# Optimization experiments

Hardware: AMD Instinct MI355X
Metric: run time of the kernel (lower is better)

## Reference

```python
import jax, jax.numpy as jnp
import numpy as np

TEXT = 226          # text_seq_length
D = 1024            # model / inner dim
HEADS = 16
HD = D // HEADS     # 64
F = 13              # latent frames
FH, FW = 8, 12      # feature h/w = H/8/2, W/8/2
ST = F * FH * FW    # 1248 spatial tokens
S = TEXT + ST       # 1474 full sequence
NEG = -1e9


def sdpa(q, k, v, bias=None):
    # q:[b,h,Q,d] k,v:[b,h,K,d]; math path of F.scaled_dot_product_attention
    scale = 1.0 / jnp.sqrt(jnp.asarray(q.shape[-1], q.dtype))
    s = jnp.einsum('bhqd,bhkd->bhqk', q, k) * scale
    if bias is not None:
        s = s + bias
    p = jax.nn.softmax(s, axis=-1)
    return jnp.einsum('bhqk,bhkd->bhqd', p, v)


def setup_inputs() -> dict:
    key = jax.random.key(0)
    ks = jax.random.split(key, 11)
    w = 0.02
    return {
        'hidden_states': jax.random.normal(ks[0], (2, ST, D), jnp.float32),
        'encoder_hidden_states': jax.random.normal(ks[1], (2, TEXT, D), jnp.float32),
        'mask': jax.random.randint(ks[2], (F, 1, FH, FW), 0, 2),  # masks_for_attn (binary)
        'wq': jax.random.normal(ks[3], (D, D), jnp.float32) * w,
        'bq': jnp.zeros((D,), jnp.float32),
        'wk': jax.random.normal(ks[4], (D, D), jnp.float32) * w,
        'bk': jnp.zeros((D,), jnp.float32),
        'wv': jax.random.normal(ks[5], (D, D), jnp.float32) * w,
        'bv': jnp.zeros((D,), jnp.float32),
        'wo': jax.random.normal(ks[6], (D, D), jnp.float32) * w,
        'bo': jnp.zeros((D,), jnp.float32),
    }


def reference(hidden_states, encoder_hidden_states, mask, wq, bq, wk, bk, wv, bv, wo, bo):
    B = hidden_states.shape[0]  # 2: [cond, uncond]
    x = jnp.concatenate([encoder_hidden_states, hidden_states], axis=1)  # [2,S,D]

    def proj(w, b):
        y = x @ w + b                                   # [2,S,D]
        return y.reshape(B, S, HEADS, HD).transpose(0, 2, 1, 3)  # [2,H,S,hd]

    q = proj(wq, bq)
    k = proj(wk, bk)
    v = proj(wv, bv)

    # chunk into cond / uncond (source)
    key_cond, source_key = k[0:1], k[1:2]
    value_cond, source_value = v[0:1], v[1:2]

    # spatio-temporal source K/V (drop text tokens)
    st_source_key = source_key[:, :, TEXT:, :]    # [1,H,ST,hd]
    st_source_value = source_value[:, :, TEXT:, :]

    # 'masked' selective attention: the torch code gathers, per frame, the
    # source tokens where masks_for_attn > 0 and concatenates them after
    # key_cond. Softmax over a gathered subset == softmax over the full
    # appended set with -inf bias on unselected positions (identical math).
    sel = (mask[:, 0] > 0).reshape(-1)            # [ST] frame-major f,h,w order
    append_bias = jnp.where(sel, 0.0, NEG).astype(q.dtype)
    bias = jnp.concatenate([jnp.zeros((S,), q.dtype), append_bias])[None, None, None, :]  # [1,1,1,S+ST]

    st_key_cond = jnp.concatenate([key_cond, st_source_key], axis=2)      # [1,H,S+ST,hd]
    st_value_cond = jnp.concatenate([value_cond, st_source_value], axis=2)

    text_q = q[0:1, :, :TEXT, :]
    st_q = q[0:1, :, TEXT:, :]

    # extend_st_for_text_keys=True: text queries also attend to extended keys
    text_hs = sdpa(text_q, st_key_cond, st_value_cond, bias)  # [1,H,TEXT,hd]
    st_hs = sdpa(st_q, st_key_cond, st_value_cond, bias)      # [1,H,ST,hd]
    cond_hs = jnp.concatenate([text_hs, st_hs], axis=2)       # [1,H,S,hd]

    uncond_hs = sdpa(q[1:2], k[1:2], v[1:2])                  # [1,H,S,hd]

    hs = jnp.concatenate([cond_hs, uncond_hs], axis=0)        # [2,H,S,hd]
    hs = hs.transpose(0, 2, 1, 3).reshape(B, S, D)
    out = hs @ wo + bo                                        # to_out[0]; to_out[1] dropout is identity in eval

    return out[:, TEXT:, :], out[:, :TEXT, :]                 # (hidden_states, encoder_hidden_states)
```

## Files before the change

kernel.cpp:

```cpp
#include <hip/hip_runtime.h>
#include <hip/hip_bf16.h>

#define TEXT_N 226
#define D_N    1024
#define HEADS_N 16
#define HD_N   64
#define ST_N   1248
#define S_N    1474
#define L0_N   2722
#define NT_C   43
#define NT_U   24
#define L0P_N  (NT_C*64)
#define SP_N   (NT_U*64)
#define M_ROWS 2948
#define MB_N   24
#define KB_N   16
#define NEGB   -1000000000.0f

typedef __hip_bfloat16 bf16_t;
typedef short s16x8 __attribute__((ext_vector_type(8)));
typedef short s16x4 __attribute__((ext_vector_type(4)));
typedef float f32x4 __attribute__((ext_vector_type(4)));

__device__ __forceinline__ f32x4 mfma16(s16x8 a, s16x8 b, f32x4 c) {
    return __builtin_amdgcn_mfma_f32_16x16x32_bf16(a, b, c, 0, 0, 0);
}

typedef __attribute__((address_space(1))) const unsigned int gu32;
typedef __attribute__((address_space(3))) unsigned int lu32;
__device__ __forceinline__ void glds16(const void* g, void* l) {
    __builtin_amdgcn_global_load_lds((gu32*)g, (lu32*)l, 16, 0, 0);
}

__device__ __forceinline__ short f2bs(float x) {
    __hip_bfloat16 h = __float2bfloat16(x);
    return *(short*)&h;
}
__device__ __forceinline__ int swz(int r, int c) {
    return r * 64 + ((((c >> 3) ^ (r & 7)) << 3) | (c & 7));
}

__global__ __launch_bounds__(256) void prep(
    const float* __restrict__ hid, const float* __restrict__ enc,
    const int* __restrict__ mask,
    const float* __restrict__ wq, const float* __restrict__ wk,
    const float* __restrict__ wv, const float* __restrict__ wo,
    bf16_t* __restrict__ wimg, bf16_t* __restrict__ xb,
    float* __restrict__ biasc, float* __restrict__ biasu) {
    __shared__ float Lw[64 * 129];
    const int b = blockIdx.x, t = threadIdx.x;
    if (b < 512) {
        const int wid = b >> 7, nblk = (b >> 4) & 7, kb = b & 15;
        const float* w = (wid == 0) ? wq : (wid == 1) ? wk : (wid == 2) ? wv : wo;
        const int k0 = kb * 64, n0 = nblk * 128;
#pragma unroll
        for (int i = 0; i < 8; i++) {
            int idx = t + i * 256;
            int kr = idx >> 5, c4 = (idx & 31) * 4;
            float4 v = *(const float4*)(w + (size_t)(k0 + kr) * D_N + n0 + c4);
            Lw[kr * 129 + c4 + 0] = v.x; Lw[kr * 129 + c4 + 1] = v.y;
            Lw[kr * 129 + c4 + 2] = v.z; Lw[kr * 129 + c4 + 3] = v.w;
        }
        __syncthreads();
        bf16_t* dst = wimg + (((size_t)wid * 8 + nblk) * 16 + kb) * 8192;
#pragma unroll
        for (int i = 0; i < 4; i++) {
            int u = t + i * 256;
            int r = u >> 3, p = u & 7;
            int ul = p ^ (r & 7);
            s16x8 o;
#pragma unroll
            for (int e = 0; e < 8; e++)
                o[e] = f2bs(Lw[(ul * 8 + e) * 129 + r]);
            *(s16x8*)(dst + r * 64 + p * 8) = o;
        }
    } else if (b < 896) {
        const int tile = b - 512;
        const int mblk = tile >> 4, kb = tile & 15;
        bf16_t* dst = xb + (size_t)tile * 8192;
#pragma unroll
        for (int i = 0; i < 4; i++) {
            int u = t + i * 256;
            int r = u >> 3, p = u & 7;
            int m = mblk * 128 + r;
            if (m >= M_ROWS) continue;
            int bb = m >= S_N; int s = m - bb * S_N;
            const float* src = (s < TEXT_N)
                ? (enc + (size_t)(bb * TEXT_N + s) * D_N)
                : (hid + (size_t)(bb * ST_N + (s - TEXT_N)) * D_N);
            int k = kb * 64 + (p ^ (r & 7)) * 8;
            float4 f0 = *(const float4*)(src + k);
            float4 f1 = *(const float4*)(src + k + 4);
            s16x8 o;
            o[0]=f2bs(f0.x); o[1]=f2bs(f0.y); o[2]=f2bs(f0.z); o[3]=f2bs(f0.w);
            o[4]=f2bs(f1.x); o[5]=f2bs(f1.y); o[6]=f2bs(f1.z); o[7]=f2bs(f1.w);
            *(s16x8*)(dst + r * 64 + p * 8) = o;
        }
    } else {
        int j = (b - 896) * 256 + t;
        if (j < L0P_N) {
            float v = 0.f;
            if (j >= L0_N) v = NEGB;
            else if (j >= S_N) v = (mask[j - S_N] > 0) ? 0.f : NEGB;
            biasc[j] = v;
        }
        int j2 = j - L0P_N;
        if (j2 >= 0 && j2 < SP_N) biasu[j2] = (j2 < S_N) ? 0.f : NEGB;
    }
}

__global__ __launch_bounds__(256) void qkv_proj(
    const bf16_t* __restrict__ xb, const bf16_t* __restrict__ wimg,
    const float* __restrict__ bq, const float* __restrict__ bk, const float* __restrict__ bv,
    bf16_t* __restrict__ Q, bf16_t* __restrict__ Kc, bf16_t* __restrict__ Ku,
    bf16_t* __restrict__ Vc, bf16_t* __restrict__ Vu) {
    __shared__ __align__(16) bf16_t As[8192];
    __shared__ __align__(16) bf16_t Bs[8192];
    const int z = blockIdx.z;
    const float* bias = (z == 0) ? bq : (z == 1) ? bk : bv;
    const int nblk = blockIdx.x, mblk = blockIdx.y;
    const int t = threadIdx.x, wave = t >> 6, lane = t & 63, ln = lane & 15, qd = lane >> 4;
    const int wm = (wave >> 1) * 64, wn = (wave & 1) * 64;
    const bf16_t* Ai = xb + (size_t)mblk * KB_N * 8192;
    const bf16_t* Bi = wimg + ((size_t)z * 8 + nblk) * KB_N * 8192;

    f32x4 acc[4][4];
    const f32x4 z4 = {0.f, 0.f, 0.f, 0.f};
#pragma unroll
    for (int mi = 0; mi < 4; mi++)
#pragma unroll
        for (int ni = 0; ni < 4; ni++) acc[mi][ni] = z4;

    for (int kb = 0; kb < KB_N; kb++) {
        const bf16_t* at = Ai + (size_t)kb * 8192;
        const bf16_t* bt = Bi + (size_t)kb * 8192;
#pragma unroll
        for (int i = 0; i < 4; i++) {
            glds16(at + (t + i * 256) * 8, As + (t + i * 256) * 8);
            glds16(bt + (t + i * 256) * 8, Bs + (t + i * 256) * 8);
        }
        __syncthreads();
#pragma unroll
        for (int kk = 0; kk < 2; kk++) {
            const int po = (((kk * 4 + qd) ^ (ln & 7)) << 3);
            s16x8 af[4], bfr[4];
#pragma unroll
            for (int mi = 0; mi < 4; mi++) af[mi]  = *(const s16x8*)(As + (wm + mi * 16 + ln) * 64 + po);
#pragma unroll
            for (int ni = 0; ni < 4; ni++) bfr[ni] = *(const s16x8*)(Bs + (wn + ni * 16 + ln) * 64 + po);
#pragma unroll
            for (int mi = 0; mi < 4; mi++)
#pragma unroll
                for (int ni = 0; ni < 4; ni++) acc[mi][ni] = mfma16(af[mi], bfr[ni], acc[mi][ni]);
        }
        __syncthreads();
    }

#pragma unroll
    for (int ni = 0; ni < 4; ni++) {
        int n = nblk * 128 + wn + ni * 16 + ln;
        float bn = bias[n];
        int h = n >> 6, d = n & 63;
#pragma unroll
        for (int mi = 0; mi < 4; mi++) {
#pragma unroll
            for (int r = 0; r < 4; r++) {
                int m = mblk * 128 + wm + mi * 16 + qd * 4 + r;
                if (m >= M_ROWS) continue;
                int b = m >= S_N; int s = m - b * S_N;
                bf16_t v = __float2bfloat16(acc[mi][ni][r] + bn);
                if (z == 0) {
                    Q[((size_t)(b * HEADS_N + h) * SP_N + s) * HD_N + d] = v;
                } else if (z == 1) {
                    if (!b) {
                        Kc[((size_t)h * NT_C + (s >> 6)) * 4096 + swz(s & 63, d)] = v;
                    } else {
                        Ku[((size_t)h * NT_U + (s >> 6)) * 4096 + swz(s & 63, d)] = v;
                        if (s >= TEXT_N) {
                            int j = S_N + s - TEXT_N;
                            Kc[((size_t)h * NT_C + (j >> 6)) * 4096 + swz(j & 63, d)] = v;
                        }
                    }
                } else {
                    if (!b) {
                        Vc[((size_t)h * NT_C + (s >> 6)) * 4096 + swz(d, s & 63)] = v;
                    } else {
                        Vu[((size_t)h * NT_U + (s >> 6)) * 4096 + swz(d, s & 63)] = v;
                        if (s >= TEXT_N) {
                            int j = S_N + s - TEXT_N;
                            Vc[((size_t)h * NT_C + (j >> 6)) * 4096 + swz(d, j & 63)] = v;
                        }
                    }
                }
            }
        }
    }
}

__global__ __launch_bounds__(256) void attn_k(
    const bf16_t* __restrict__ Q, const bf16_t* __restrict__ Kc, const bf16_t* __restrict__ Ku,
    const bf16_t* __restrict__ Vc, const bf16_t* __restrict__ Vu,
    const float* __restrict__ biasc, const float* __restrict__ biasu,
    bf16_t* __restrict__ hs) {
    __shared__ __align__(16) bf16_t Ks[4096];
    __shared__ __align__(16) bf16_t Vs[4096];
    __shared__ __align__(16) bf16_t Ps[4][1024];
    __shared__ __align__(16) float  bsL[L0P_N];
    const int cs = blockIdx.z, h = blockIdx.y, q0 = blockIdx.x * 64;
    const int nt = cs ? NT_U : NT_C;
    const bf16_t* Ki = cs ? (Ku + (size_t)h * NT_U * 4096) : (Kc + (size_t)h * NT_C * 4096);
    const bf16_t* Vi = cs ? (Vu + (size_t)h * NT_U * 4096) : (Vc + (size_t)h * NT_C * 4096);
    const float* bsrc = cs ? biasu : biasc;
    const int t = threadIdx.x, wave = t >> 6, lane = t & 63, ln = lane & 15, qd = lane >> 4;
    const int q = q0 + wave * 16 + ln;

    for (int i = t * 4; i < nt * 64; i += 1024)
        *(float4*)(bsL + i) = *(const float4*)(bsrc + i);

    const bf16_t* Qp = Q + ((size_t)(cs * HEADS_N + h) * SP_N + q) * HD_N;
    s16x8 qf[2];
    qf[0] = *(const s16x8*)(Qp + qd * 8);
    qf[1] = *(const s16x8*)(Qp + 32 + qd * 8);

    f32x4 o[4];
    const f32x4 z4 = {0.f, 0.f, 0.f, 0.f};
#pragma unroll
    for (int mi = 0; mi < 4; mi++) o[mi] = z4;
    float m_r = -1e30f, l_r = 0.f;
    bf16_t* pw = (bf16_t*)Ps[wave];

    for (int kt = 0; kt < nt; kt++) {
        const bf16_t* kp = Ki + (size_t)kt * 4096;
        const bf16_t* vp = Vi + (size_t)kt * 4096;
#pragma unroll
        for (int i = 0; i < 2; i++) {
            glds16(kp + (t + i * 256) * 8, Ks + (t + i * 256) * 8);
            glds16(vp + (t + i * 256) * 8, Vs + (t + i * 256) * 8);
        }
        __syncthreads();

        f32x4 st[4];
#pragma unroll
        for (int ni = 0; ni < 4; ni++) st[ni] = z4;
#pragma unroll
        for (int kk = 0; kk < 2; kk++) {
            const int po = (((kk * 4 + qd) ^ (ln & 7)) << 3);
#pragma unroll
            for (int ni = 0; ni < 4; ni++) {
                s16x8 kf = *(const s16x8*)(Ks + (ni * 16 + ln) * 64 + po);
                st[ni] = mfma16(kf, qf[kk], st[ni]);
            }
        }
        float mloc = -1e30f;
#pragma unroll
        for (int ni = 0; ni < 4; ni++) {
            f32x4 bv4 = *(const f32x4*)(bsL + kt * 64 + ni * 16 + qd * 4);
#pragma unroll
            for (int r = 0; r < 4; r++) {
                st[ni][r] = st[ni][r] * 0.125f + bv4[r];
                mloc = fmaxf(mloc, st[ni][r]);
            }
        }
        mloc = fmaxf(mloc, __shfl_xor(mloc, 16));
        mloc = fmaxf(mloc, __shfl_xor(mloc, 32));
        float mn = fmaxf(m_r, mloc);
        float alpha = __expf(m_r - mn);
        m_r = mn;
        float rs = 0.f;
#pragma unroll
        for (int ni = 0; ni < 4; ni++)
#pragma unroll
            for (int r = 0; r < 4; r++) {
                float p = __expf(st[ni][r] - mn);
                st[ni][r] = p;
                rs += p;
            }
        rs += __shfl_xor(rs, 16);
        rs += __shfl_xor(rs, 32);
        l_r = l_r * alpha + rs;
#pragma unroll
        for (int ni = 0; ni < 4; ni++) {
            s16x4 pk;
            pk[0] = f2bs(st[ni][0]); pk[1] = f2bs(st[ni][1]);
            pk[2] = f2bs(st[ni][2]); pk[3] = f2bs(st[ni][3]);
            int c0 = ni * 16 + qd * 4;
            *(s16x4*)(pw + ln * 64 + ((((c0 >> 3) ^ (ln & 7)) << 3) | (c0 & 7))) = pk;
        }
#pragma unroll
        for (int mi = 0; mi < 4; mi++) {
            o[mi][0] *= alpha; o[mi][1] *= alpha; o[mi][2] *= alpha; o[mi][3] *= alpha;
        }
        asm volatile("s_waitcnt lgkmcnt(0)" ::: "memory");
#pragma unroll
        for (int kk = 0; kk < 2; kk++) {
            const int po = (((kk * 4 + qd) ^ (ln & 7)) << 3);
            s16x8 pb = *(const s16x8*)(pw + ln * 64 + po);
#pragma unroll
            for (int mi = 0; mi < 4; mi++) {
                s16x8 vf = *(const s16x8*)(Vs + (mi * 16 + ln) * 64 + po);
                o[mi] = mfma16(vf, pb, o[mi]);
            }
        }
        __syncthreads();
    }
    if (q < S_N) {
        float inv = 1.f / l_r;
        int m = cs * S_N + q;
        bf16_t* dst = hs + ((size_t)(m >> 7) * 16 + h) * 8192;
        int r = m & 127;
#pragma unroll
        for (int mi = 0; mi < 4; mi++) {
            s16x4 ov;
            ov[0] = f2bs(o[mi][0] * inv); ov[1] = f2bs(o[mi][1] * inv);
            ov[2] = f2bs(o[mi][2] * inv); ov[3] = f2bs(o[mi][3] * inv);
            int c0 = mi * 16 + qd * 4;
            *(s16x4*)(dst + r * 64 + ((((c0 >> 3) ^ (r & 7)) << 3) | (c0 & 7))) = ov;
        }
    }
}

__global__ __launch_bounds__(256) void out_proj(
    const bf16_t* __restrict__ hsi, const bf16_t* __restrict__ wimg,
    const float* __restrict__ bo, float* __restrict__ out) {
    __shared__ __align__(16) bf16_t As[8192];
    __shared__ __align__(16) bf16_t Bs[8192];
    const int nblk = blockIdx.x, mblk = blockIdx.y;
    const int t = threadIdx.x, wave = t >> 6, lane = t & 63, ln = lane & 15, qd = lane >> 4;
    const int wm = (wave >> 1) * 64, wn = (wave & 1) * 64;
    const bf16_t* Ai = hsi + (size_t)mblk * KB_N * 8192;
    const bf16_t* Bi = wimg + ((size_t)3 * 8 + nblk) * KB_N * 8192;

    f32x4 acc[4][4];
    const f32x4 z4 = {0.f, 0.f, 0.f, 0.f};
#pragma unroll
    for (int mi = 0; mi < 4; mi++)
#pragma unroll
        for (int ni = 0; ni < 4; ni++) acc[mi][ni] = z4;

    for (int kb = 0; kb < KB_N; kb++) {
        const bf16_t* at = Ai + (size_t)kb * 8192;
        const bf16_t* bt = Bi + (size_t)kb * 8192;
#pragma unroll
        for (int i = 0; i < 4; i++) {
            glds16(at + (t + i * 256) * 8, As + (t + i * 256) * 8);
            glds16(bt + (t + i * 256) * 8, Bs + (t + i * 256) * 8);
        }
        __syncthreads();
#pragma unroll
        for (int kk = 0; kk < 2; kk++) {
            const int po = (((kk * 4 + qd) ^ (ln & 7)) << 3);
            s16x8 af[4], bfr[4];
#pragma unroll
            for (int mi = 0; mi < 4; mi++) af[mi]  = *(const s16x8*)(As + (wm + mi * 16 + ln) * 64 + po);
#pragma unroll
            for (int ni = 0; ni < 4; ni++) bfr[ni] = *(const s16x8*)(Bs + (wn + ni * 16 + ln) * 64 + po);
#pragma unroll
            for (int mi = 0; mi < 4; mi++)
#pragma unroll
                for (int ni = 0; ni < 4; ni++) acc[mi][ni] = mfma16(af[mi], bfr[ni], acc[mi][ni]);
        }
        __syncthreads();
    }
#pragma unroll
    for (int ni = 0; ni < 4; ni++) {
        int n = nblk * 128 + wn + ni * 16 + ln;
        float bn = bo[n];
#pragma unroll
        for (int mi = 0; mi < 4; mi++) {
#pragma unroll
            for (int r = 0; r < 4; r++) {
                int m = mblk * 128 + wm + mi * 16 + qd * 4 + r;
                if (m >= M_ROWS) continue;
                int b = m >= S_N; int s = m - b * S_N;
                float v = acc[mi][ni][r] + bn;
                size_t off = (s >= TEXT_N)
                    ? ((size_t)(b * ST_N + (s - TEXT_N)) * D_N + n)
                    : ((size_t)2 * ST_N * D_N + (size_t)(b * TEXT_N + s) * D_N + n);
                out[off] = v;
            }
        }
    }
}

extern "C" void kernel_launch(void* const* d_in, const int* in_sizes, int n_in,
                              void* d_out, int out_size, void* d_ws, size_t ws_size,
                              hipStream_t stream) {
    const float* hid = (const float*)d_in[0];
    const float* enc = (const float*)d_in[1];
    const int*  mask = (const int*)d_in[2];
    const float* wq = (const float*)d_in[3];
    const float* bq = (const float*)d_in[4];
    const float* wk = (const float*)d_in[5];
    const float* bk = (const float*)d_in[6];
    const float* wv = (const float*)d_in[7];
    const float* bv = (const float*)d_in[8];
    const float* wo = (const float*)d_in[9];
    const float* bo = (const float*)d_in[10];

    bf16_t* w = (bf16_t*)d_ws;
    const size_t WIMG = (size_t)4 * 8 * 16 * 8192;
    const size_t XIMG = (size_t)MB_N * KB_N * 8192;
    bf16_t* wimg = w;
    bf16_t* xb   = wimg + WIMG;
    bf16_t* Qb   = xb + XIMG;
    bf16_t* Kc   = Qb + (size_t)2 * HEADS_N * SP_N * HD_N;
    bf16_t* Ku   = Kc + (size_t)HEADS_N * NT_C * 4096;
    bf16_t* Vc   = Ku + (size_t)HEADS_N * NT_U * 4096;
    bf16_t* Vu   = Vc + (size_t)HEADS_N * NT_C * 4096;
    float*  biasf = (float*)(Vu + (size_t)HEADS_N * NT_U * 4096);
    float*  biasc = biasf;
    float*  biasu = biasf + L0P_N;
    bf16_t* hsi  = xb;

    prep<<<913, 256, 0, stream>>>(hid, enc, mask, wq, wk, wv, wo, wimg, xb, biasc, biasu);
    qkv_proj<<<dim3(8, MB_N, 3), 256, 0, stream>>>(xb, wimg, bq, bk, bv, Qb, Kc, Ku, Vc, Vu);
    attn_k<<<dim3(24, 16, 2), 256, 0, stream>>>(Qb, Kc, Ku, Vc, Vu, biasc, biasu, hsi);
    out_proj<<<dim3(8, MB_N), 256, 0, stream>>>(hsi, wimg, bo, (float*)d_out);
}
```

Baseline: 226.1 us.

## Pad batch rows, share K image, vectorize V stores, skip redundant softmax rescale

Rows of the two batches are padded to 1536 each so tiles never straddle the cond/uncond boundary. K is stored once per batch in a row-swizzled image, and the cond attention loads the extended source keys straight from the uncond image instead of from a duplicate. V stores from the projection epilogue become packed 4-wide writes. The attention kernel drops the LDS bias staging and applies the bias only on tail tiles, skips the online-softmax rescale when no row max changes, uses a flattened 1D grid with cond/uncond interleaved, and replaces the bf16 conversion with a manual round-to-nearest bit trick. Together these cut global write traffic and per-tile ALU work, at the cost of more branching and extra per-lane address computation in the K loads.

Result: slower. 245.7 us (+8.7%).

```diff
diff --git a/kernel.cpp b/kernel.cpp
--- a/kernel.cpp
+++ b/kernel.cpp
@@ -11,8 +11,7 @@
 #define NT_C   43
 #define NT_U   24
 #define L0P_N  (NT_C*64)
-#define SP_N   (NT_U*64)
-#define M_ROWS 2948
+#define SP_N   1536
 #define MB_N   24
 #define KB_N   16
 #define NEGB   -1000000000.0f
@@ -33,8 +32,9 @@
 }
 
 __device__ __forceinline__ short f2bs(float x) {
-    __hip_bfloat16 h = __float2bfloat16(x);
-    return *(short*)&h;
+    unsigned u = __float_as_uint(x);
+    u += 0x7FFF + ((u >> 16) & 1);
+    return (short)(u >> 16);
 }
 __device__ __forceinline__ int swz(int r, int c) {
     return r * 64 + ((((c >> 3) ^ (r & 7)) << 3) | (c & 7));
@@ -83,8 +83,8 @@
             int u = t + i * 256;
             int r = u >> 3, p = u & 7;
             int m = mblk * 128 + r;
-            if (m >= M_ROWS) continue;
-            int bb = m >= S_N; int s = m - bb * S_N;
+            int bb = m >= SP_N; int s = m - bb * SP_N;
+            if (s >= S_N) continue;
             const float* src = (s < TEXT_N)
                 ? (enc + (size_t)(bb * TEXT_N + s) * D_N)
                 : (hid + (size_t)(bb * ST_N + (s - TEXT_N)) * D_N);
@@ -112,7 +112,7 @@
 __global__ __launch_bounds__(256) void qkv_proj(
     const bf16_t* __restrict__ xb, const bf16_t* __restrict__ wimg,
     const float* __restrict__ bq, const float* __restrict__ bk, const float* __restrict__ bv,
-    bf16_t* __restrict__ Q, bf16_t* __restrict__ Kc, bf16_t* __restrict__ Ku,
+    bf16_t* __restrict__ Q, bf16_t* __restrict__ Kimg,
     bf16_t* __restrict__ Vc, bf16_t* __restrict__ Vu) {
     __shared__ __align__(16) bf16_t As[8192];
     __shared__ __align__(16) bf16_t Bs[8192];
@@ -161,61 +161,89 @@
         int n = nblk * 128 + wn + ni * 16 + ln;
         float bn = bias[n];
         int h = n >> 6, d = n & 63;
-#pragma unroll
-        for (int mi = 0; mi < 4; mi++) {
-#pragma unroll
-            for (int r = 0; r < 4; r++) {
-                int m = mblk * 128 + wm + mi * 16 + qd * 4 + r;
-                if (m >= M_ROWS) continue;
-                int b = m >= S_N; int s = m - b * S_N;
-                bf16_t v = __float2bfloat16(acc[mi][ni][r] + bn);
-                if (z == 0) {
-                    Q[((size_t)(b * HEADS_N + h) * SP_N + s) * HD_N + d] = v;
-                } else if (z == 1) {
-                    if (!b) {
-                        Kc[((size_t)h * NT_C + (s >> 6)) * 4096 + swz(s & 63, d)] = v;
+        if (z == 2) {
+#pragma unroll
+            for (int mi = 0; mi < 4; mi++) {
+                int mb4 = mblk * 128 + wm + mi * 16 + qd * 4;
+                int b = mb4 >= SP_N; int s = mb4 - b * SP_N;
+                if (s >= S_N) continue;
+                s16x4 pk;
+#pragma unroll
+                for (int r = 0; r < 4; r++) pk[r] = f2bs(acc[mi][ni][r] + bn);
+                bool full = (s + 3 < S_N);
+                if (!b) {
+                    if (full) {
+                        *(s16x4*)(Vc + ((size_t)h * NT_C + (s >> 6)) * 4096 + swz(d, s & 63)) = pk;
                     } else {
-                        Ku[((size_t)h * NT_U + (s >> 6)) * 4096 + swz(s & 63, d)] = v;
-                        if (s >= TEXT_N) {
-                            int j = S_N + s - TEXT_N;
-                            Kc[((size_t)h * NT_C + (j >> 6)) * 4096 + swz(j & 63, d)] = v;
-                        }
+                        for (int r = 0; r < 4; r++)
+                            if (s + r < S_N)
+                                *(short*)&Vc[((size_t)h * NT_C + ((s + r) >> 6)) * 4096 + swz(d, (s + r) & 63)] = pk[r];
                     }
                 } else {
-                    if (!b) {
-                        Vc[((size_t)h * NT_C + (s >> 6)) * 4096 + swz(d, s & 63)] = v;
+                    if (full) {
+                        *(s16x4*)(Vu + ((size_t)h * NT_U + (s >> 6)) * 4096 + swz(d, s & 63)) = pk;
+                        if (s >= TEXT_N) {
+                            int j = s + 1248;
+                            *(s16x4*)(Vc + ((size_t)h * NT_C + (j >> 6)) * 4096 + swz(d, j & 63)) = pk;
+                        } else if (s + 3 >= TEXT_N) {
+                            for (int r = 0; r < 4; r++)
+                                if (s + r >= TEXT_N) {
+                                    int j = s + r + 1248;
+                                    *(short*)&Vc[((size_t)h * NT_C + (j >> 6)) * 4096 + swz(d, j & 63)] = pk[r];
+                                }
+                        }
                     } else {
-                        Vu[((size_t)h * NT_U + (s >> 6)) * 4096 + swz(d, s & 63)] = v;
-                        if (s >= TEXT_N) {
-                            int j = S_N + s - TEXT_N;
-                            Vc[((size_t)h * NT_C + (j >> 6)) * 4096 + swz(d, j & 63)] = v;
-                        }
+                        for (int r = 0; r < 4; r++)
+                            if (s + r < S_N) {
+                                *(short*)&Vu[((size_t)h * NT_U + ((s + r) >> 6)) * 4096 + swz(d, (s + r) & 63)] = pk[r];
+                                if (s + r >= TEXT_N) {
+                                    int j = s + r + 1248;
+                                    *(short*)&Vc[((size_t)h * NT_C + (j >> 6)) * 4096 + swz(d, j & 63)] = pk[r];
+                                }
+                            }
                     }
                 }
             }
+        } else {
+#pragma unroll
+            for (int mi = 0; mi < 4; mi++) {
+#pragma unroll
+                for (int r = 0; r < 4; r++) {
+                    int m = mblk * 128 + wm + mi * 16 + qd * 4 + r;
+                    int b = m >= SP_N; int s = m - b * SP_N;
+                    if (s >= S_N) continue;
+                    float fv = acc[mi][ni][r] + bn;
+                    short v = f2bs(fv);
+                    if (z == 0) {
+                        *(short*)&Q[((size_t)(b * HEADS_N + h) * SP_N + s) * HD_N + d] = v;
+                    } else {
+                        *(short*)&Kimg[((size_t)(b * HEADS_N + h) * SP_N + s) * 64 +
+                             ((((d >> 3) ^ (s & 7)) << 3) | (d & 7))] = v;
+                    }
+                }
+            }
         }
     }
 }
 
 __global__ __launch_bounds__(256) void attn_k(
-    const bf16_t* __restrict__ Q, const bf16_t* __restrict__ Kc, const bf16_t* __restrict__ Ku,
+    const bf16_t* __restrict__ Q, const bf16_t* __restrict__ Kimg,
     const bf16_t* __restrict__ Vc, const bf16_t* __restrict__ Vu,
     const float* __restrict__ biasc, const float* __restrict__ biasu,
     bf16_t* __restrict__ hs) {
     __shared__ __align__(16) bf16_t Ks[4096];
     __shared__ __align__(16) bf16_t Vs[4096];
     __shared__ __align__(16) bf16_t Ps[4][1024];
-    __shared__ __align__(16) float  bsL[L0P_N];
-    const int cs = blockIdx.z, h = blockIdx.y, q0 = blockIdx.x * 64;
+    const int bid = blockIdx.x;
+    const int cs = bid & 1, h = (bid >> 1) & 15, q0 = (bid >> 5) * 64;
     const int nt = cs ? NT_U : NT_C;
-    const bf16_t* Ki = cs ? (Ku + (size_t)h * NT_U * 4096) : (Kc + (size_t)h * NT_C * 4096);
+    const float* bsrc = cs ? biasu : biasc;
+    const bf16_t* K0 = Kimg + (size_t)h * SP_N * 64;
+    const bf16_t* K1 = Kimg + (size_t)(HEADS_N + h) * SP_N * 64;
+    const bf16_t* Kb = cs ? K1 : K0;
     const bf16_t* Vi = cs ? (Vu + (size_t)h * NT_U * 4096) : (Vc + (size_t)h * NT_C * 4096);
-    const float* bsrc = cs ? biasu : biasc;
     const int t = threadIdx.x, wave = t >> 6, lane = t & 63, ln = lane & 15, qd = lane >> 4;
     const int q = q0 + wave * 16 + ln;
-
-    for (int i = t * 4; i < nt * 64; i += 1024)
-        *(float4*)(bsL + i) = *(const float4*)(bsrc + i);
 
     const bf16_t* Qp = Q + ((size_t)(cs * HEADS_N + h) * SP_N + q) * HD_N;
     s16x8 qf[2];
@@ -230,12 +258,16 @@
     bf16_t* pw = (bf16_t*)Ps[wave];
 
     for (int kt = 0; kt < nt; kt++) {
-        const bf16_t* kp = Ki + (size_t)kt * 4096;
-        const bf16_t* vp = Vi + (size_t)kt * 4096;
+        const int j0 = kt * 64;
+        const bf16_t* vt = Vi + (size_t)kt * 4096;
 #pragma unroll
         for (int i = 0; i < 2; i++) {
-            glds16(kp + (t + i * 256) * 8, Ks + (t + i * 256) * 8);
-            glds16(vp + (t + i * 256) * 8, Vs + (t + i * 256) * 8);
+            int u = t + i * 256, r_l = u >> 3, p = u & 7;
+            int j = j0 + r_l;
+            const bf16_t* krow = (!cs && j >= S_N) ? (K1 + (size_t)(j - 1248) * 64)
+                                                   : (Kb + (size_t)j * 64);
+            glds16(krow + p * 8, Ks + u * 8);
+            glds16(vt + u * 8, Vs + u * 8);
         }
         __syncthreads();
 
@@ -252,32 +284,49 @@
             }
         }
         float mloc = -1e30f;
-#pragma unroll
-        for (int ni = 0; ni < 4; ni++) {
-            f32x4 bv4 = *(const f32x4*)(bsL + kt * 64 + ni * 16 + qd * 4);
-#pragma unroll
-            for (int r = 0; r < 4; r++) {
-                st[ni][r] = st[ni][r] * 0.125f + bv4[r];
-                mloc = fmaxf(mloc, st[ni][r]);
-            }
+        if (j0 + 64 > S_N) {
+#pragma unroll
+            for (int ni = 0; ni < 4; ni++) {
+                f32x4 bv4 = *(const f32x4*)(bsrc + j0 + ni * 16 + qd * 4);
+#pragma unroll
+                for (int r = 0; r < 4; r++) {
+                    st[ni][r] = st[ni][r] * 0.125f + bv4[r];
+                    mloc = fmaxf(mloc, st[ni][r]);
+                }
+            }
+        } else {
+#pragma unroll
+            for (int ni = 0; ni < 4; ni++)
+#pragma unroll
+                for (int r = 0; r < 4; r++) {
+                    st[ni][r] *= 0.125f;
+                    mloc = fmaxf(mloc, st[ni][r]);
+                }
         }
         mloc = fmaxf(mloc, __shfl_xor(mloc, 16));
         mloc = fmaxf(mloc, __shfl_xor(mloc, 32));
         float mn = fmaxf(m_r, mloc);
-        float alpha = __expf(m_r - mn);
-        m_r = mn;
+        if (__any(mn > m_r)) {
+            float alpha = __expf(m_r - mn);
+            m_r = mn;
+            l_r *= alpha;
+#pragma unroll
+            for (int mi = 0; mi < 4; mi++) {
+                o[mi][0] *= alpha; o[mi][1] *= alpha; o[mi][2] *= alpha; o[mi][3] *= alpha;
+            }
+        }
         float rs = 0.f;
 #pragma unroll
         for (int ni = 0; ni < 4; ni++)
 #pragma unroll
             for (int r = 0; r < 4; r++) {
-                float p = __expf(st[ni][r] - mn);
+                float p = __expf(st[ni][r] - m_r);
                 st[ni][r] = p;
                 rs += p;
             }
         rs += __shfl_xor(rs, 16);
         rs += __shfl_xor(rs, 32);
-        l_r = l_r * alpha + rs;
+        l_r += rs;
 #pragma unroll
         for (int ni = 0; ni < 4; ni++) {
             s16x4 pk;
@@ -286,10 +335,6 @@
             int c0 = ni * 16 + qd * 4;
             *(s16x4*)(pw + ln * 64 + ((((c0 >> 3) ^ (ln & 7)) << 3) | (c0 & 7))) = pk;
         }
-#pragma unroll
-        for (int mi = 0; mi < 4; mi++) {
-            o[mi][0] *= alpha; o[mi][1] *= alpha; o[mi][2] *= alpha; o[mi][3] *= alpha;
-        }
         asm volatile("s_waitcnt lgkmcnt(0)" ::: "memory");
 #pragma unroll
         for (int kk = 0; kk < 2; kk++) {
@@ -305,7 +350,7 @@
     }
     if (q < S_N) {
         float inv = 1.f / l_r;
-        int m = cs * S_N + q;
+        int m = cs * SP_N + q;
         bf16_t* dst = hs + ((size_t)(m >> 7) * 16 + h) * 8192;
         int r = m & 127;
 #pragma unroll
@@ -370,8 +415,8 @@
 #pragma unroll
             for (int r = 0; r < 4; r++) {
                 int m = mblk * 128 + wm + mi * 16 + qd * 4 + r;
-                if (m >= M_ROWS) continue;
-                int b = m >= S_N; int s = m - b * S_N;
+                int b = m >= SP_N; int s = m - b * SP_N;
+                if (s >= S_N) continue;
                 float v = acc[mi][ni][r] + bn;
                 size_t off = (s >= TEXT_N)
                     ? ((size_t)(b * ST_N + (s - TEXT_N)) * D_N + n)
@@ -403,17 +448,15 @@
     bf16_t* wimg = w;
     bf16_t* xb   = wimg + WIMG;
     bf16_t* Qb   = xb + XIMG;
-    bf16_t* Kc   = Qb + (size_t)2 * HEADS_N * SP_N * HD_N;
-    bf16_t* Ku   = Kc + (size_t)HEADS_N * NT_C * 4096;
-    bf16_t* Vc   = Ku + (size_t)HEADS_N * NT_U * 4096;
+    bf16_t* Kimg = Qb + (size_t)2 * HEADS_N * SP_N * HD_N;
+    bf16_t* Vc   = Kimg + (size_t)2 * HEADS_N * SP_N * 64;
     bf16_t* Vu   = Vc + (size_t)HEADS_N * NT_C * 4096;
-    float*  biasf = (float*)(Vu + (size_t)HEADS_N * NT_U * 4096);
-    float*  biasc = biasf;
-    float*  biasu = biasf + L0P_N;
+    float*  biasc = (float*)(Vu + (size_t)HEADS_N * NT_U * 4096);
+    float*  biasu = biasc + L0P_N;
     bf16_t* hsi  = xb;
 
     prep<<<913, 256, 0, stream>>>(hid, enc, mask, wq, wk, wv, wo, wimg, xb, biasc, biasu);
-    qkv_proj<<<dim3(8, MB_N, 3), 256, 0, stream>>>(xb, wimg, bq, bk, bv, Qb, Kc, Ku, Vc, Vu);
-    attn_k<<<dim3(24, 16, 2), 256, 0, stream>>>(Qb, Kc, Ku, Vc, Vu, biasc, biasu, hsi);
+    qkv_proj<<<dim3(8, MB_N, 3), 256, 0, stream>>>(xb, wimg, bq, bk, bv, Qb, Kimg, Vc, Vu);
+    attn_k<<<768, 256, 0, stream>>>(Qb, Kimg, Vc, Vu, biasc, biasu, hsi);
     out_proj<<<dim3(8, MB_N), 256, 0, stream>>>(hsi, wimg, bo, (float*)d_out);
 }
```
